# Optimization experiments

Hardware: AMD Instinct MI355X
Metric: run time of the kernel (lower is better)

Reference implementation:

```python
import jax, jax.numpy as jnp
import numpy as np

BS = 256          # batch_size
NN = BS - 1
D = 128           # projection dim
SIGMA = 0.07      # rbf gamma (self.sigma)
C = 1.0
REG = 0.1
NUM_ITERS = 1000
ETA = 0.001
USE_NORM = True


def setup_inputs() -> dict:
    key = jax.random.key(0)
    k1, k2 = jax.random.split(key)
    z = jax.random.normal(k1, (BS, 2, D), dtype=jnp.float32)
    alpha_init = jax.random.normal(k2, (BS, NN, 1), dtype=jnp.float32)
    return {"z": z, "alpha_init": alpha_init}


def _rbf_kernel(X, Y, gamma):
    # exp(-gamma * ||x - y||^2)
    xn = jnp.sum(X * X, axis=1, keepdims=True)          # [n,1]
    yn = jnp.sum(Y * Y, axis=1, keepdims=True).T        # [1,m]
    d = xn + yn - 2.0 * (X @ Y.T)
    return jnp.exp(-gamma * d)


def _pgd_nesterov(DD, p, alpha0, eta, num_iters, C, use_norm):
    # minimize 0.5 a'DDa - p'a  s.t. 0 <= a <= C, batched over bs
    def step(carry, t):
        alpha, alpha_prev = carry
        beta = t / (t + 3.0)
        y = alpha + beta * (alpha - alpha_prev)
        grad = jnp.einsum('bij,bjk->bik', DD, y) - p     # [bs,nn,1]
        if use_norm:
            grad = grad / (jnp.linalg.norm(grad, axis=1, keepdims=True) + 1e-12)
        alpha_new = jnp.clip(y - eta * grad, 0.0, C)
        return (alpha_new, alpha), None
    (alpha, _), _ = jax.lax.scan(step, (alpha0, alpha0),
                                 jnp.arange(num_iters, dtype=jnp.float32))
    return alpha


def reference(z, alpha_init):
    bs, nn = BS, NN
    # F.normalize(z, p=2, dim=1): normalize over the view axis (faithful to source)
    nrm = jnp.maximum(jnp.linalg.norm(z, axis=1, keepdims=True), 1e-12)
    ftr = z / nrm
    ftr = jnp.concatenate([ftr[:, 0, :], ftr[:, 1, :]], axis=0)   # [2bs, d]

    K = _rbf_kernel(ftr[:bs], ftr, SIGMA)                          # [bs, 2bs]

    # ---- QP construction + solve under no_grad ----
    Kd = jax.lax.stop_gradient(K)
    KK = Kd[:, :bs]                                                # block: first bs cols
    r = jnp.arange(bs)
    m = jnp.arange(nn)
    # idx[i] = [0..bs-1] without i  (KMASK row/col removal)
    idx = m[None, :] + (m[None, :] >= r[:, None]).astype(jnp.int32)  # [bs, nn]
    KK_sub = KK[idx[:, :, None], idx[:, None, :]]                  # [bs,nn,nn]
    row = jnp.take_along_axis(KK, idx, axis=1)                     # row[i,m]=KK[i,idx[i,m]]
    # Delta[i,j,k] = 1 + reg*d_jk + KK[j,k] - KK[i,j] - KK[i,k]  (j,k != i)
    DD = (1.0 + REG * jnp.eye(nn, dtype=KK.dtype)[None]
          + KK_sub - row[:, :, None] - row[:, None, :])            # [bs,nn,nn]

    p = 2.0 * jnp.ones((bs, nn, 1), dtype=jnp.float32)
    alpha0 = jnp.clip(jax.nn.relu(alpha_init), 0.0, C)
    alpha = _pgd_nesterov(DD, p, alpha0, ETA, NUM_ITERS, C, USE_NORM)
    alpha_y = jnp.clip(jax.nn.relu(alpha[:, :, 0]), 0.0, C)
    alpha_y = jax.lax.stop_gradient(alpha_y)                       # [bs,nn]
    alpha_x = alpha_y.sum(axis=1)                                  # [bs]

    # ---- loss terms (grad flows through K here) ----
    Ks = K[:, bs:]                                                 # block12: [bs,bs]
    # Kn.T[i,m] = Ks.T[i, idx[i,m]]  (neg_mask = off-diagonal)
    KnT = jnp.take_along_axis(Ks.T, idx, axis=1)                   # [bs,nn]
    pos = jnp.diagonal(Ks)                                         # pos_mask = eye
    pos_loss = jnp.mean(alpha_x * pos)
    neg_loss = jnp.sum(alpha_y * KnT) / bs
    loss = neg_loss - pos_loss

    sparsity = ((alpha_y == C).sum().astype(jnp.float32)
                / ((alpha_y > 0).sum().astype(jnp.float32) + 1e-10))
    num_zero = (alpha_y == 0.0).mean()
    return (loss, pos.mean(), KnT.mean(), sparsity, num_zero, jnp.float32(0.0))
```

## Files before the change

### kernel.cpp

```cpp
#include <hip/hip_runtime.h>
#include <math.h>

#define BS   256
#define NN   255
#define DIM  128
#define GAMMA 0.07
#define NUM_ITERS 1000

__device__ __forceinline__ double wred_d(double v) {
  #pragma unroll
  for (int k = 1; k < 64; k <<= 1) v += __shfl_xor(v, k, 64);
  return v;
}
__device__ __forceinline__ int wred_i(int v) {
  #pragma unroll
  for (int k = 1; k < 64; k <<= 1) v += __shfl_xor(v, k, 64);
  return v;
}

__device__ __forceinline__ float RLF(float v, int lane) {
  return __int_as_float(__builtin_amdgcn_readlane(__float_as_int(v), lane));
}

template <int CTRL, int RMASK>
__device__ __forceinline__ float dpp_add(float x) {
  int t = __builtin_amdgcn_update_dpp(0, __float_as_int(x), CTRL, RMASK, 0xf, true);
  return x + __int_as_float(t);
}
__device__ __forceinline__ float wred64_dpp(float x) {
  x = dpp_add<0x111, 0xf>(x);
  x = dpp_add<0x112, 0xf>(x);
  x = dpp_add<0x114, 0xf>(x);
  x = dpp_add<0x118, 0xf>(x);
  x = dpp_add<0x142, 0xa>(x);
  x = dpp_add<0x143, 0xc>(x);
  return RLF(x, 63);
}

__device__ __forceinline__ float rsq_nr(float x) {
  float r;
  asm("v_rsq_f32 %0, %1" : "=v"(r) : "v"(x));
  r = r * (1.5f - 0.5f * x * r * r);
  return r;
}

__device__ __forceinline__ float4 add4(float4 a, float4 b) {
  float4 c; c.x = a.x + b.x; c.y = a.y + b.y; c.z = a.z + b.z; c.w = a.w + b.w;
  return c;
}

__global__ void k_ftr(const float* __restrict__ z, double* __restrict__ ftrT) {
  int b = blockIdx.x;
  int d = threadIdx.x;
  double z0 = (double)z[b * 256 + d];
  double z1 = (double)z[b * 256 + 128 + d];
  double n = sqrt(z0 * z0 + z1 * z1);
  n = fmax(n, 1e-12);
  ftrT[d * 512 + b]       = z0 / n;
  ftrT[d * 512 + 256 + b] = z1 / n;
}

__global__ void k_K(const double* __restrict__ ftrT, float* __restrict__ K,
                    double* __restrict__ pk_knt, double* __restrict__ pos_arr) {
  int i = blockIdx.x;
  int t = threadIdx.x;
  __shared__ double rowi[DIM];
  __shared__ double redd[4];
  if (t < DIM) rowi[t] = ftrT[t * 512 + i];
  __syncthreads();
  double xn = 0.0;
  #pragma unroll 8
  for (int d = 0; d < DIM; ++d) xn += rowi[d] * rowi[d];

  double knt_part = 0.0;
  #pragma unroll
  for (int h = 0; h < 2; ++h) {
    int j = t + h * 256;
    double dot = 0.0, sq = 0.0;
    #pragma unroll 8
    for (int d = 0; d < DIM; ++d) {
      double f = ftrT[d * 512 + j];
      dot += rowi[d] * f;
      sq  += f * f;
    }
    double dist = xn + sq - 2.0 * dot;
    double kv = exp(-GAMMA * dist);
    K[i * 512 + j] = (float)kv;
    if (h == 1) {
      if (j == 256 + i) pos_arr[i] = kv;
      else knt_part += kv;
    }
  }
  double w = wred_d(knt_part);
  if ((t & 63) == 0) redd[t >> 6] = w;
  __syncthreads();
  if (t == 0) pk_knt[i] = redd[0] + redd[1] + redd[2] + redd[3];
}

__global__ __launch_bounds__(512, 2) void k_pgd(
    const float* __restrict__ K, const float* __restrict__ alpha_init,
    double* __restrict__ neg_arr, double* __restrict__ sa_arr,
    int* __restrict__ cnt1, int* __restrict__ cntp, int* __restrict__ cnt0) {
  int r = blockIdx.x;
  int tid = threadIdx.x;
  int l = tid & 63;
  int rg = tid >> 6;

  __shared__ __align__(16) float ytil[BS];
  __shared__ __align__(16) float part[8][BS];
  __shared__ float S_lds[1];
  __shared__ float betat[1024];

  for (int i = tid; i < 1024; i += 512)
    betat[i] = (float)i / ((float)i + 3.0f);

  float4 kq[32];
  #pragma unroll
  for (int j = 0; j < 32; ++j)
    kq[j] = *(const float4*)&K[(32 * rg + j) * 512 + 4 * l];
  #pragma unroll
  for (int j = 0; j < 32; ++j)
    asm volatile("" : "+v"(kq[j].x), "+v"(kq[j].y), "+v"(kq[j].z), "+v"(kq[j].w));

  float al[4], ap[4], yv[4], kv[4], rm2[4];
  if (rg == 0) {
    #pragma unroll
    for (int k = 0; k < 4; ++k) {
      int a = 4 * l + k;
      if (a == r) {
        al[k] = 0.f; ap[k] = 0.f; yv[k] = 0.f; kv[k] = 0.f; rm2[k] = 0.f;
      } else {
        int c = a - (a > r ? 1 : 0);
        float v = alpha_init[r * NN + c];
        v = fminf(fmaxf(v, 0.f), 1.f);
        al[k] = v; ap[k] = v; yv[k] = v;
        kv[k] = 1.0f - K[r * 512 + a];
        rm2[k] = 2.0f;
      }
    }
    float4 y4 = {yv[0], yv[1], yv[2], yv[3]};
    *(float4*)&ytil[4 * l] = y4;
  }
  __syncthreads();

  int rq = r >> 2, rc = r & 3;

  for (int it = 0; it < NUM_ITERS; ++it) {
    if (rg == 1) {
      float4 yq = *(const float4*)&ytil[4 * l];
      float Sv = wred64_dpp((yq.x + yq.y) + (yq.z + yq.w));
      if (l == 0) S_lds[0] = Sv;
    }
    const float4* yb = (const float4*)&ytil[32 * rg];
    float4 acc = {0.f, 0.f, 0.f, 0.f};
    #pragma unroll
    for (int jj = 0; jj < 8; ++jj) {
      float4 yq = yb[jj];
      float4 k0 = kq[4 * jj + 0], k1 = kq[4 * jj + 1];
      float4 k2 = kq[4 * jj + 2], k3 = kq[4 * jj + 3];
      acc.x = fmaf(k0.x, yq.x, acc.x); acc.y = fmaf(k0.y, yq.x, acc.y);
      acc.z = fmaf(k0.z, yq.x, acc.z); acc.w = fmaf(k0.w, yq.x, acc.w);
      acc.x = fmaf(k1.x, yq.y, acc.x); acc.y = fmaf(k1.y, yq.y, acc.y);
      acc.z = fmaf(k1.z, yq.y, acc.z); acc.w = fmaf(k1.w, yq.y, acc.w);
      acc.x = fmaf(k2.x, yq.z, acc.x); acc.y = fmaf(k2.y, yq.z, acc.y);
      acc.z = fmaf(k2.z, yq.z, acc.z); acc.w = fmaf(k2.w, yq.z, acc.w);
      acc.x = fmaf(k3.x, yq.w, acc.x); acc.y = fmaf(k3.y, yq.w, acc.y);
      acc.z = fmaf(k3.z, yq.w, acc.z); acc.w = fmaf(k3.w, yq.w, acc.w);
    }
    *(float4*)&part[rg][4 * l] = acc;
    __syncthreads();

    if (rg == 0) {
      float4 q0 = *(const float4*)&part[0][4 * l];
      float4 q1 = *(const float4*)&part[1][4 * l];
      float4 q2 = *(const float4*)&part[2][4 * l];
      float4 q3 = *(const float4*)&part[3][4 * l];
      float4 q4 = *(const float4*)&part[4][4 * l];
      float4 q5 = *(const float4*)&part[5][4 * l];
      float4 q6 = *(const float4*)&part[6][4 * l];
      float4 q7 = *(const float4*)&part[7][4 * l];
      float4 gA = add4(add4(add4(q0, q1), add4(q2, q3)),
                       add4(add4(q4, q5), add4(q6, q7)));
      float grv = (rc == 0) ? gA.x : (rc == 1) ? gA.y : (rc == 2) ? gA.z : gA.w;
      float gr = RLF(grv, rq);
      float Sv = S_lds[0];
      float beta = betat[it + 1];
      float g[4];
      g[0] = (gA.x - gr) - rm2[0] + kv[0] * Sv + 0.1f * yv[0];
      g[1] = (gA.y - gr) - rm2[1] + kv[1] * Sv + 0.1f * yv[1];
      g[2] = (gA.z - gr) - rm2[2] + kv[2] * Sv + 0.1f * yv[2];
      g[3] = (gA.w - gr) - rm2[3] + kv[3] * Sv + 0.1f * yv[3];
      float n2 = wred64_dpp((g[0] * g[0] + g[1] * g[1]) + (g[2] * g[2] + g[3] * g[3]));
      float sinv = 0.001f * rsq_nr(n2);
      #pragma unroll
      for (int k = 0; k < 4; ++k) {
        float na = fminf(fmaxf(fmaf(-sinv, g[k], yv[k]), 0.f), 1.f);
        ap[k] = al[k];
        al[k] = na;
        yv[k] = fmaf(beta, na - ap[k], na);
      }
      float4 y4 = {yv[0], yv[1], yv[2], yv[3]};
      *(float4*)&ytil[4 * l] = y4;
    }
    __syncthreads();
  }

  if (rg == 0) {
    double nl = 0.0, sa = 0.0;
    int c1 = 0, cp = 0, cz = 0;
    #pragma unroll
    for (int k = 0; k < 4; ++k) {
      int a = 4 * l + k;
      if (a != r) {
        float kx = K[a * 512 + 256 + r];
        nl += (double)al[k] * (double)kx;
        sa += (double)al[k];
        c1 += (al[k] == 1.0f);
        cp += (al[k] > 0.0f);
        cz += (al[k] == 0.0f);
      }
    }
    nl = wred_d(nl); sa = wred_d(sa);
    c1 = wred_i(c1); cp = wred_i(cp); cz = wred_i(cz);
    if (l == 0) {
      neg_arr[r] = nl;
      sa_arr[r]  = sa;
      cnt1[r] = c1; cntp[r] = cp; cnt0[r] = cz;
    }
  }
}

__global__ void k_fin(const double* __restrict__ pk_knt, const double* __restrict__ pos_arr,
                      const double* __restrict__ neg_arr, const double* __restrict__ sa_arr,
                      const int* __restrict__ cnt1, const int* __restrict__ cntp,
                      const int* __restrict__ cnt0, float* __restrict__ out) {
  int t = threadIdx.x;
  __shared__ double rd[16];
  __shared__ int ri[12];
  double knt = pk_knt[t];
  double pos = pos_arr[t];
  double neg = neg_arr[t];
  double pl  = sa_arr[t] * pos_arr[t];
  int a1 = cnt1[t], ap = cntp[t], a0 = cnt0[t];
  knt = wred_d(knt); pos = wred_d(pos); neg = wred_d(neg); pl = wred_d(pl);
  a1 = wred_i(a1); ap = wred_i(ap); a0 = wred_i(a0);
  int w = t >> 6;
  if ((t & 63) == 0) {
    rd[w] = knt; rd[4 + w] = pos; rd[8 + w] = neg; rd[12 + w] = pl;
    ri[w] = a1; ri[4 + w] = ap; ri[8 + w] = a0;
  }
  __syncthreads();
  if (t == 0) {
    double kntS = rd[0] + rd[1] + rd[2] + rd[3];
    double posS = rd[4] + rd[5] + rd[6] + rd[7];
    double negS = rd[8] + rd[9] + rd[10] + rd[11];
    double plS  = rd[12] + rd[13] + rd[14] + rd[15];
    int c1t = ri[0] + ri[1] + ri[2] + ri[3];
    int cpt = ri[4] + ri[5] + ri[6] + ri[7];
    int c0t = ri[8] + ri[9] + ri[10] + ri[11];
    out[0] = (float)(negS / 256.0 - plS / 256.0);
    out[1] = (float)(posS / 256.0);
    out[2] = (float)(kntS / (256.0 * 255.0));
    out[3] = (float)c1t / ((float)cpt + 1e-10f);
    out[4] = (float)c0t / 65280.0f;
    out[5] = 0.0f;
  }
}

extern "C" void kernel_launch(void* const* d_in, const int* in_sizes, int n_in,
                              void* d_out, int out_size, void* d_ws, size_t ws_size,
                              hipStream_t stream) {
  const float* z     = (const float*)d_in[0];
  const float* ainit = (const float*)d_in[1];
  char* ws = (char*)d_ws;
  double* ftrT   = (double*)ws;
  float*  K      = (float*)(ws + 524288);
  double* pk_knt = (double*)(ws + 1048576);
  double* pos_a  = (double*)(ws + 1048576 + 2048);
  double* neg_a  = (double*)(ws + 1048576 + 4096);
  double* sa_a   = (double*)(ws + 1048576 + 6144);
  int* cnt1 = (int*)(ws + 1048576 + 8192);
  int* cntp = (int*)(ws + 1048576 + 8192 + 1024);
  int* cnt0 = (int*)(ws + 1048576 + 8192 + 2048);
  float* out = (float*)d_out;

  k_ftr<<<256, 128, 0, stream>>>(z, ftrT);
  k_K  <<<256, 256, 0, stream>>>(ftrT, K, pk_knt, pos_a);
  k_pgd<<<256, 512, 0, stream>>>(K, ainit, neg_a, sa_a, cnt1, cntp, cnt0);
  k_fin<<<1, 256, 0, stream>>>(pk_knt, pos_a, neg_a, sa_a, cnt1, cntp, cnt0, out);
}
```

Before: 831.6 us.

## Use packed FP32 FMA for matvec and LDS atomics for cross-wave reduction

The register-resident K tile is rearranged into float2 pairs so the per-iteration matrix-vector product uses v_pk_fma_f32, issuing two FMAs per instruction. The eight-way partial-sum buffer and its reduction by wave 0 are replaced with LDS float atomicAdds into a double-buffered accumulator, which is zeroed one iteration ahead. This aims to cut VALU instruction count and the serial reduction on the critical path. In exchange it adds LDS atomic contention across eight waves and makes the float summation order nondeterministic.

```diff
diff --git a/kernel.cpp b/kernel.cpp
--- a/kernel.cpp
+++ b/kernel.cpp
@@ -6,6 +6,8 @@
 #define DIM  128
 #define GAMMA 0.07
 #define NUM_ITERS 1000
+
+typedef float v2f __attribute__((ext_vector_type(2)));
 
 __device__ __forceinline__ double wred_d(double v) {
   #pragma unroll
@@ -44,9 +46,8 @@
   return r;
 }
 
-__device__ __forceinline__ float4 add4(float4 a, float4 b) {
-  float4 c; c.x = a.x + b.x; c.y = a.y + b.y; c.z = a.z + b.z; c.w = a.w + b.w;
-  return c;
+__device__ __forceinline__ void pk_fma(v2f& acc, const v2f& k, const v2f& y) {
+  asm("v_pk_fma_f32 %0, %1, %2, %0" : "+v"(acc) : "v"(k), "v"(y));
 }
 
 __global__ void k_ftr(const float* __restrict__ z, double* __restrict__ ftrT) {
@@ -107,20 +108,26 @@
   int rg = tid >> 6;
 
   __shared__ __align__(16) float ytil[BS];
-  __shared__ __align__(16) float part[8][BS];
+  __shared__ __align__(16) float part[2][BS];
   __shared__ float S_lds[1];
   __shared__ float betat[1024];
 
   for (int i = tid; i < 1024; i += 512)
     betat[i] = (float)i / ((float)i + 3.0f);
 
-  float4 kq[32];
-  #pragma unroll
-  for (int j = 0; j < 32; ++j)
-    kq[j] = *(const float4*)&K[(32 * rg + j) * 512 + 4 * l];
-  #pragma unroll
-  for (int j = 0; j < 32; ++j)
-    asm volatile("" : "+v"(kq[j].x), "+v"(kq[j].y), "+v"(kq[j].z), "+v"(kq[j].w));
+  v2f kq[64];
+  #pragma unroll
+  for (int j = 0; j < 16; ++j) {
+    float4 r0 = *(const float4*)&K[(32 * rg + 2 * j + 0) * 512 + 4 * l];
+    float4 r1 = *(const float4*)&K[(32 * rg + 2 * j + 1) * 512 + 4 * l];
+    kq[j].x      = r0.x; kq[j].y      = r1.x;
+    kq[16 + j].x = r0.y; kq[16 + j].y = r1.y;
+    kq[32 + j].x = r0.z; kq[32 + j].y = r1.z;
+    kq[48 + j].x = r0.w; kq[48 + j].y = r1.w;
+  }
+  #pragma unroll
+  for (int j = 0; j < 64; ++j)
+    asm volatile("" : "+v"(kq[j]));
 
   float al[4], ap[4], yv[4], kv[4], rm2[4];
   if (rg == 0) {
@@ -141,46 +148,45 @@
     float4 y4 = {yv[0], yv[1], yv[2], yv[3]};
     *(float4*)&ytil[4 * l] = y4;
   }
+  {
+    float4 z4 = {0.f, 0.f, 0.f, 0.f};
+    if (l < 8) *(float4*)&part[0][32 * rg + 4 * l] = z4;
+  }
   __syncthreads();
 
   int rq = r >> 2, rc = r & 3;
 
   for (int it = 0; it < NUM_ITERS; ++it) {
+    int b = it & 1;
     if (rg == 1) {
       float4 yq = *(const float4*)&ytil[4 * l];
       float Sv = wred64_dpp((yq.x + yq.y) + (yq.z + yq.w));
       if (l == 0) S_lds[0] = Sv;
     }
+    {
+      float4 z4 = {0.f, 0.f, 0.f, 0.f};
+      if (l < 8) *(float4*)&part[b ^ 1][32 * rg + 4 * l] = z4;
+    }
     const float4* yb = (const float4*)&ytil[32 * rg];
-    float4 acc = {0.f, 0.f, 0.f, 0.f};
+    v2f a0 = {0.f, 0.f}, a1 = {0.f, 0.f}, a2 = {0.f, 0.f}, a3 = {0.f, 0.f};
     #pragma unroll
     for (int jj = 0; jj < 8; ++jj) {
       float4 yq = yb[jj];
-      float4 k0 = kq[4 * jj + 0], k1 = kq[4 * jj + 1];
-      float4 k2 = kq[4 * jj + 2], k3 = kq[4 * jj + 3];
-      acc.x = fmaf(k0.x, yq.x, acc.x); acc.y = fmaf(k0.y, yq.x, acc.y);
-      acc.z = fmaf(k0.z, yq.x, acc.z); acc.w = fmaf(k0.w, yq.x, acc.w);
-      acc.x = fmaf(k1.x, yq.y, acc.x); acc.y = fmaf(k1.y, yq.y, acc.y);
-      acc.z = fmaf(k1.z, yq.y, acc.z); acc.w = fmaf(k1.w, yq.y, acc.w);
-      acc.x = fmaf(k2.x, yq.z, acc.x); acc.y = fmaf(k2.y, yq.z, acc.y);
-      acc.z = fmaf(k2.z, yq.z, acc.z); acc.w = fmaf(k2.w, yq.z, acc.w);
-      acc.x = fmaf(k3.x, yq.w, acc.x); acc.y = fmaf(k3.y, yq.w, acc.y);
-      acc.z = fmaf(k3.z, yq.w, acc.z); acc.w = fmaf(k3.w, yq.w, acc.w);
-    }
-    *(float4*)&part[rg][4 * l] = acc;
+      v2f ylo = {yq.x, yq.y};
+      v2f yhi = {yq.z, yq.w};
+      pk_fma(a0, kq[2 * jj],     ylo); pk_fma(a0, kq[2 * jj + 1],      yhi);
+      pk_fma(a1, kq[16 + 2 * jj], ylo); pk_fma(a1, kq[16 + 2 * jj + 1], yhi);
+      pk_fma(a2, kq[32 + 2 * jj], ylo); pk_fma(a2, kq[32 + 2 * jj + 1], yhi);
+      pk_fma(a3, kq[48 + 2 * jj], ylo); pk_fma(a3, kq[48 + 2 * jj + 1], yhi);
+    }
+    atomicAdd(&part[b][4 * l + 0], a0.x + a0.y);
+    atomicAdd(&part[b][4 * l + 1], a1.x + a1.y);
+    atomicAdd(&part[b][4 * l + 2], a2.x + a2.y);
+    atomicAdd(&part[b][4 * l + 3], a3.x + a3.y);
     __syncthreads();
 
     if (rg == 0) {
-      float4 q0 = *(const float4*)&part[0][4 * l];
-      float4 q1 = *(const float4*)&part[1][4 * l];
-      float4 q2 = *(const float4*)&part[2][4 * l];
-      float4 q3 = *(const float4*)&part[3][4 * l];
-      float4 q4 = *(const float4*)&part[4][4 * l];
-      float4 q5 = *(const float4*)&part[5][4 * l];
-      float4 q6 = *(const float4*)&part[6][4 * l];
-      float4 q7 = *(const float4*)&part[7][4 * l];
-      float4 gA = add4(add4(add4(q0, q1), add4(q2, q3)),
-                       add4(add4(q4, q5), add4(q6, q7)));
+      float4 gA = *(const float4*)&part[b][4 * l];
       float grv = (rc == 0) ? gA.x : (rc == 1) ? gA.y : (rc == 2) ? gA.z : gA.w;
       float gr = RLF(grv, rq);
       float Sv = S_lds[0];
```

Result: slower. 3.222 ms (+287.4%).

## Replicate PGD update across all waves to drop second barrier per iteration

Applied to the files above, without the earlier changes.

Each of the eight wavefronts now performs the gradient reduction, norm and Nesterov update redundantly, so every wave holds the full y vector in registers. Each wave writes only its own slice of y into a per-wave LDS buffer, and the partial-product buffer is double-buffered. Together these remove the second __syncthreads per iteration. The running sum S is computed locally with a wave reduction instead of by a separate wave through LDS. Launch bounds drop to one block per SIMD group, which frees registers but lowers occupancy, and redundant ALU work is added in every wave.

```diff
diff --git a/kernel.cpp b/kernel.cpp
--- a/kernel.cpp
+++ b/kernel.cpp
@@ -97,7 +97,7 @@
   if (t == 0) pk_knt[i] = redd[0] + redd[1] + redd[2] + redd[3];
 }
 
-__global__ __launch_bounds__(512, 2) void k_pgd(
+__global__ __launch_bounds__(512, 1) void k_pgd(
     const float* __restrict__ K, const float* __restrict__ alpha_init,
     double* __restrict__ neg_arr, double* __restrict__ sa_arr,
     int* __restrict__ cnt1, int* __restrict__ cntp, int* __restrict__ cnt0) {
@@ -106,9 +106,8 @@
   int l = tid & 63;
   int rg = tid >> 6;
 
-  __shared__ __align__(16) float ytil[BS];
-  __shared__ __align__(16) float part[8][BS];
-  __shared__ float S_lds[1];
+  __shared__ __align__(16) float ytw[8][32];
+  __shared__ __align__(16) float part[2][8][BS];
   __shared__ float betat[1024];
 
   for (int i = tid; i < 1024; i += 512)
@@ -123,39 +122,35 @@
     asm volatile("" : "+v"(kq[j].x), "+v"(kq[j].y), "+v"(kq[j].z), "+v"(kq[j].w));
 
   float al[4], ap[4], yv[4], kv[4], rm2[4];
-  if (rg == 0) {
-    #pragma unroll
-    for (int k = 0; k < 4; ++k) {
-      int a = 4 * l + k;
-      if (a == r) {
-        al[k] = 0.f; ap[k] = 0.f; yv[k] = 0.f; kv[k] = 0.f; rm2[k] = 0.f;
-      } else {
-        int c = a - (a > r ? 1 : 0);
-        float v = alpha_init[r * NN + c];
-        v = fminf(fmaxf(v, 0.f), 1.f);
-        al[k] = v; ap[k] = v; yv[k] = v;
-        kv[k] = 1.0f - K[r * 512 + a];
-        rm2[k] = 2.0f;
-      }
-    }
+  #pragma unroll
+  for (int k = 0; k < 4; ++k) {
+    int a = 4 * l + k;
+    if (a == r) {
+      al[k] = 0.f; ap[k] = 0.f; yv[k] = 0.f; kv[k] = 0.f; rm2[k] = 0.f;
+    } else {
+      int c = a - (a > r ? 1 : 0);
+      float v = alpha_init[r * NN + c];
+      v = fminf(fmaxf(v, 0.f), 1.f);
+      al[k] = v; ap[k] = v; yv[k] = v;
+      kv[k] = 1.0f - K[r * 512 + a];
+      rm2[k] = 2.0f;
+    }
+  }
+  float S = wred64_dpp((yv[0] + yv[1]) + (yv[2] + yv[3]));
+  if ((l >> 3) == rg) {
     float4 y4 = {yv[0], yv[1], yv[2], yv[3]};
-    *(float4*)&ytil[4 * l] = y4;
+    *(float4*)&ytw[rg][4 * (l & 7)] = y4;
   }
   __syncthreads();
 
   int rq = r >> 2, rc = r & 3;
 
   for (int it = 0; it < NUM_ITERS; ++it) {
-    if (rg == 1) {
-      float4 yq = *(const float4*)&ytil[4 * l];
-      float Sv = wred64_dpp((yq.x + yq.y) + (yq.z + yq.w));
-      if (l == 0) S_lds[0] = Sv;
-    }
-    const float4* yb = (const float4*)&ytil[32 * rg];
+    int b = it & 1;
     float4 acc = {0.f, 0.f, 0.f, 0.f};
     #pragma unroll
     for (int jj = 0; jj < 8; ++jj) {
-      float4 yq = yb[jj];
+      float4 yq = *(const float4*)&ytw[rg][4 * jj];
       float4 k0 = kq[4 * jj + 0], k1 = kq[4 * jj + 1];
       float4 k2 = kq[4 * jj + 2], k3 = kq[4 * jj + 3];
       acc.x = fmaf(k0.x, yq.x, acc.x); acc.y = fmaf(k0.y, yq.x, acc.y);
@@ -167,42 +162,43 @@
       acc.x = fmaf(k3.x, yq.w, acc.x); acc.y = fmaf(k3.y, yq.w, acc.y);
       acc.z = fmaf(k3.z, yq.w, acc.z); acc.w = fmaf(k3.w, yq.w, acc.w);
     }
-    *(float4*)&part[rg][4 * l] = acc;
+    *(float4*)&part[b][rg][4 * l] = acc;
     __syncthreads();
 
-    if (rg == 0) {
-      float4 q0 = *(const float4*)&part[0][4 * l];
-      float4 q1 = *(const float4*)&part[1][4 * l];
-      float4 q2 = *(const float4*)&part[2][4 * l];
-      float4 q3 = *(const float4*)&part[3][4 * l];
-      float4 q4 = *(const float4*)&part[4][4 * l];
-      float4 q5 = *(const float4*)&part[5][4 * l];
-      float4 q6 = *(const float4*)&part[6][4 * l];
-      float4 q7 = *(const float4*)&part[7][4 * l];
-      float4 gA = add4(add4(add4(q0, q1), add4(q2, q3)),
-                       add4(add4(q4, q5), add4(q6, q7)));
-      float grv = (rc == 0) ? gA.x : (rc == 1) ? gA.y : (rc == 2) ? gA.z : gA.w;
-      float gr = RLF(grv, rq);
-      float Sv = S_lds[0];
-      float beta = betat[it + 1];
-      float g[4];
-      g[0] = (gA.x - gr) - rm2[0] + kv[0] * Sv + 0.1f * yv[0];
-      g[1] = (gA.y - gr) - rm2[1] + kv[1] * Sv + 0.1f * yv[1];
-      g[2] = (gA.z - gr) - rm2[2] + kv[2] * Sv + 0.1f * yv[2];
-      g[3] = (gA.w - gr) - rm2[3] + kv[3] * Sv + 0.1f * yv[3];
-      float n2 = wred64_dpp((g[0] * g[0] + g[1] * g[1]) + (g[2] * g[2] + g[3] * g[3]));
-      float sinv = 0.001f * rsq_nr(n2);
-      #pragma unroll
-      for (int k = 0; k < 4; ++k) {
-        float na = fminf(fmaxf(fmaf(-sinv, g[k], yv[k]), 0.f), 1.f);
-        ap[k] = al[k];
-        al[k] = na;
-        yv[k] = fmaf(beta, na - ap[k], na);
-      }
+    float4 q0 = *(const float4*)&part[b][0][4 * l];
+    float4 q1 = *(const float4*)&part[b][1][4 * l];
+    float4 q2 = *(const float4*)&part[b][2][4 * l];
+    float4 q3 = *(const float4*)&part[b][3][4 * l];
+    float4 q4 = *(const float4*)&part[b][4][4 * l];
+    float4 q5 = *(const float4*)&part[b][5][4 * l];
+    float4 q6 = *(const float4*)&part[b][6][4 * l];
+    float4 q7 = *(const float4*)&part[b][7][4 * l];
+    float4 gA = add4(add4(add4(q0, q1), add4(q2, q3)),
+                     add4(add4(q4, q5), add4(q6, q7)));
+    float grv = (rc == 0) ? gA.x : (rc == 1) ? gA.y : (rc == 2) ? gA.z : gA.w;
+    float gr = RLF(grv, rq);
+    float beta = betat[it + 1];
+    float g[4];
+    g[0] = (gA.x - gr) - rm2[0] + kv[0] * S + 0.1f * yv[0];
+    g[1] = (gA.y - gr) - rm2[1] + kv[1] * S + 0.1f * yv[1];
+    g[2] = (gA.z - gr) - rm2[2] + kv[2] * S + 0.1f * yv[2];
+    g[3] = (gA.w - gr) - rm2[3] + kv[3] * S + 0.1f * yv[3];
+    float n2 = wred64_dpp((g[0] * g[0] + g[1] * g[1]) + (g[2] * g[2] + g[3] * g[3]));
+    float sinv = 0.001f * rsq_nr(n2);
+    float ysum = 0.f;
+    #pragma unroll
+    for (int k = 0; k < 4; ++k) {
+      float na = fminf(fmaxf(fmaf(-sinv, g[k], yv[k]), 0.f), 1.f);
+      ap[k] = al[k];
+      al[k] = na;
+      yv[k] = fmaf(beta, na - ap[k], na);
+      ysum += yv[k];
+    }
+    S = wred64_dpp(ysum);
+    if ((l >> 3) == rg) {
       float4 y4 = {yv[0], yv[1], yv[2], yv[3]};
-      *(float4*)&ytil[4 * l] = y4;
-    }
-    __syncthreads();
+      *(float4*)&ytw[rg][4 * (l & 7)] = y4;
+    }
   }
 
   if (rg == 0) {
```

Measured after the change: 935.7 us. 1.13x slower.

## Spread PGD gradient reduction and update across all eight waves

Applied to the files above, without the earlier changes.

Previously wave 0 alone reduced the eight partial matvec rows and updated all 256 alpha entries while the other waves idled. Now each wave reduces and updates its own 32-column slice, with wave-local partial sums for S and the gradient norm shared through LDS. Each wave reads only its own slice of ytil in the matvec, so ytil is updated without cross-wave hazards. The cost is one extra block barrier per iteration for the norm reduction, plus lanes 32-63 idling during the update; the part array is padded to 264 to avoid LDS bank conflicts.

```diff
diff --git a/kernel.cpp b/kernel.cpp
--- a/kernel.cpp
+++ b/kernel.cpp
@@ -42,11 +42,6 @@
   asm("v_rsq_f32 %0, %1" : "=v"(r) : "v"(x));
   r = r * (1.5f - 0.5f * x * r * r);
   return r;
-}
-
-__device__ __forceinline__ float4 add4(float4 a, float4 b) {
-  float4 c; c.x = a.x + b.x; c.y = a.y + b.y; c.z = a.z + b.z; c.w = a.w + b.w;
-  return c;
 }
 
 __global__ void k_ftr(const float* __restrict__ z, double* __restrict__ ftrT) {
@@ -97,7 +92,7 @@
   if (t == 0) pk_knt[i] = redd[0] + redd[1] + redd[2] + redd[3];
 }
 
-__global__ __launch_bounds__(512, 2) void k_pgd(
+__global__ __launch_bounds__(512, 1) void k_pgd(
     const float* __restrict__ K, const float* __restrict__ alpha_init,
     double* __restrict__ neg_arr, double* __restrict__ sa_arr,
     int* __restrict__ cnt1, int* __restrict__ cntp, int* __restrict__ cnt0) {
@@ -107,9 +102,12 @@
   int rg = tid >> 6;
 
   __shared__ __align__(16) float ytil[BS];
-  __shared__ __align__(16) float part[8][BS];
-  __shared__ float S_lds[1];
+  __shared__ __align__(16) float part[8][264];
+  __shared__ __align__(16) float Sp[8];
+  __shared__ __align__(16) float n2p[8];
   __shared__ float betat[1024];
+  __shared__ double eNL[8], eSA[8];
+  __shared__ int eC1[8], eCP[8], eCZ[8];
 
   for (int i = tid; i < 1024; i += 512)
     betat[i] = (float)i / ((float)i + 3.0f);
@@ -122,35 +120,28 @@
   for (int j = 0; j < 32; ++j)
     asm volatile("" : "+v"(kq[j].x), "+v"(kq[j].y), "+v"(kq[j].z), "+v"(kq[j].w));
 
-  float al[4], ap[4], yv[4], kv[4], rm2[4];
-  if (rg == 0) {
-    #pragma unroll
-    for (int k = 0; k < 4; ++k) {
-      int a = 4 * l + k;
-      if (a == r) {
-        al[k] = 0.f; ap[k] = 0.f; yv[k] = 0.f; kv[k] = 0.f; rm2[k] = 0.f;
-      } else {
-        int c = a - (a > r ? 1 : 0);
-        float v = alpha_init[r * NN + c];
-        v = fminf(fmaxf(v, 0.f), 1.f);
-        al[k] = v; ap[k] = v; yv[k] = v;
-        kv[k] = 1.0f - K[r * 512 + a];
-        rm2[k] = 2.0f;
-      }
-    }
-    float4 y4 = {yv[0], yv[1], yv[2], yv[3]};
-    *(float4*)&ytil[4 * l] = y4;
-  }
-  __syncthreads();
-
-  int rq = r >> 2, rc = r & 3;
+  int a = 32 * rg + l;
+  float alS = 0.f, apS = 0.f, yvS = 0.f, kvS = 0.f, m = 0.f;
+  if (l < 32) {
+    if (a != r) {
+      int c = a - (a > r ? 1 : 0);
+      float v = alpha_init[r * NN + c];
+      v = fminf(fmaxf(v, 0.f), 1.f);
+      alS = v; apS = v; yvS = v;
+      kvS = 1.0f - K[r * 512 + a];
+      m = 1.f;
+    }
+    ytil[a] = yvS;
+  }
+  {
+    float ys = wred64_dpp(yvS);
+    if (l == 0) Sp[rg] = ys;
+  }
+  __syncthreads();
 
   for (int it = 0; it < NUM_ITERS; ++it) {
-    if (rg == 1) {
-      float4 yq = *(const float4*)&ytil[4 * l];
-      float Sv = wred64_dpp((yq.x + yq.y) + (yq.z + yq.w));
-      if (l == 0) S_lds[0] = Sv;
-    }
+    float beta = betat[it + 1];
+
     const float4* yb = (const float4*)&ytil[32 * rg];
     float4 acc = {0.f, 0.f, 0.f, 0.f};
     #pragma unroll
@@ -170,63 +161,66 @@
     *(float4*)&part[rg][4 * l] = acc;
     __syncthreads();
 
-    if (rg == 0) {
-      float4 q0 = *(const float4*)&part[0][4 * l];
-      float4 q1 = *(const float4*)&part[1][4 * l];
-      float4 q2 = *(const float4*)&part[2][4 * l];
-      float4 q3 = *(const float4*)&part[3][4 * l];
-      float4 q4 = *(const float4*)&part[4][4 * l];
-      float4 q5 = *(const float4*)&part[5][4 * l];
-      float4 q6 = *(const float4*)&part[6][4 * l];
-      float4 q7 = *(const float4*)&part[7][4 * l];
-      float4 gA = add4(add4(add4(q0, q1), add4(q2, q3)),
-                       add4(add4(q4, q5), add4(q6, q7)));
-      float grv = (rc == 0) ? gA.x : (rc == 1) ? gA.y : (rc == 2) ? gA.z : gA.w;
-      float gr = RLF(grv, rq);
-      float Sv = S_lds[0];
-      float beta = betat[it + 1];
-      float g[4];
-      g[0] = (gA.x - gr) - rm2[0] + kv[0] * Sv + 0.1f * yv[0];
-      g[1] = (gA.y - gr) - rm2[1] + kv[1] * Sv + 0.1f * yv[1];
-      g[2] = (gA.z - gr) - rm2[2] + kv[2] * Sv + 0.1f * yv[2];
-      g[3] = (gA.w - gr) - rm2[3] + kv[3] * Sv + 0.1f * yv[3];
-      float n2 = wred64_dpp((g[0] * g[0] + g[1] * g[1]) + (g[2] * g[2] + g[3] * g[3]));
-      float sinv = 0.001f * rsq_nr(n2);
-      #pragma unroll
-      for (int k = 0; k < 4; ++k) {
-        float na = fminf(fmaxf(fmaf(-sinv, g[k], yv[k]), 0.f), 1.f);
-        ap[k] = al[k];
-        al[k] = na;
-        yv[k] = fmaf(beta, na - ap[k], na);
-      }
-      float4 y4 = {yv[0], yv[1], yv[2], yv[3]};
-      *(float4*)&ytil[4 * l] = y4;
-    }
+    int cc = 32 * rg + (l & 31);
+    int b0 = (l >> 5) * 4;
+    float s01 = part[b0 + 0][cc] + part[b0 + 1][cc];
+    float s23 = part[b0 + 2][cc] + part[b0 + 3][cc];
+    float gh = s01 + s23;
+    float gA = gh + __shfl_down(gh, 32, 64);
+
+    float grp = (l < 8) ? part[l][r] : 0.f;
+    grp += __shfl_down(grp, 4, 64);
+    grp += __shfl_down(grp, 2, 64);
+    grp += __shfl_down(grp, 1, 64);
+    float gr = RLF(grp, 0);
+
+    float4 sA = *(const float4*)&Sp[0];
+    float4 sB = *(const float4*)&Sp[4];
+    float S = ((sA.x + sA.y) + (sA.z + sA.w)) + ((sB.x + sB.y) + (sB.z + sB.w));
+
+    float g = ((gA - gr) - 2.0f * m + kvS * S + 0.1f * yvS) * m;
+    float n2part = wred64_dpp(g * g);
+    if (l == 0) n2p[rg] = n2part;
     __syncthreads();
-  }
-
-  if (rg == 0) {
+
+    float4 nA = *(const float4*)&n2p[0];
+    float4 nB = *(const float4*)&n2p[4];
+    float n2 = ((nA.x + nA.y) + (nA.z + nA.w)) + ((nB.x + nB.y) + (nB.z + nB.w));
+    float sinv = 0.001f * rsq_nr(n2);
+    float na = fminf(fmaxf(fmaf(-sinv, g, yvS), 0.f), 1.f);
+    apS = alS; alS = na;
+    yvS = fmaf(beta, na - apS, na);
+    if (l < 32) ytil[a] = yvS;
+    float ys = wred64_dpp(yvS);
+    if (l == 0) Sp[rg] = ys;
+  }
+
+  {
     double nl = 0.0, sa = 0.0;
     int c1 = 0, cp = 0, cz = 0;
-    #pragma unroll
-    for (int k = 0; k < 4; ++k) {
-      int a = 4 * l + k;
-      if (a != r) {
-        float kx = K[a * 512 + 256 + r];
-        nl += (double)al[k] * (double)kx;
-        sa += (double)al[k];
-        c1 += (al[k] == 1.0f);
-        cp += (al[k] > 0.0f);
-        cz += (al[k] == 0.0f);
-      }
+    if (l < 32 && a != r) {
+      float kx = K[a * 512 + 256 + r];
+      nl = (double)alS * (double)kx;
+      sa = (double)alS;
+      c1 = (alS == 1.0f);
+      cp = (alS > 0.0f);
+      cz = (alS == 0.0f);
     }
     nl = wred_d(nl); sa = wred_d(sa);
     c1 = wred_i(c1); cp = wred_i(cp); cz = wred_i(cz);
-    if (l == 0) {
-      neg_arr[r] = nl;
-      sa_arr[r]  = sa;
-      cnt1[r] = c1; cntp[r] = cp; cnt0[r] = cz;
-    }
+    if (l == 0) { eNL[rg] = nl; eSA[rg] = sa; eC1[rg] = c1; eCP[rg] = cp; eCZ[rg] = cz; }
+  }
+  __syncthreads();
+  if (tid == 0) {
+    double nlS = 0.0, saS = 0.0; int c1S = 0, cpS = 0, czS = 0;
+    #pragma unroll
+    for (int k = 0; k < 8; ++k) {
+      nlS += eNL[k]; saS += eSA[k];
+      c1S += eC1[k]; cpS += eCP[k]; czS += eCZ[k];
+    }
+    neg_arr[r] = nlS;
+    sa_arr[r]  = saS;
+    cnt1[r] = c1S; cntp[r] = cpS; cnt0[r] = czS;
   }
 }
 
```

New measurement: 1.035 ms. +24.4%, slower.
